# Kernel tuning notes

Measured on AMD Instinct MI355X. Metric: run time of the kernel, lower is better.

## Reference

```python
import jax, jax.numpy as jnp
import numpy as np

N, E, D, L, G, C = 20000, 320000, 512, 6, 64, 10
EPS = 1e-5


def setup_inputs() -> dict:
    key = jax.random.key(0)
    ks = jax.random.split(key, 8)
    s = 0.05  # small init scale to keep activations sane across 6 layers
    x = jax.random.normal(ks[0], (N, D), jnp.float32)
    edge_index = jax.random.randint(ks[1], (2, E), 0, N, jnp.int32)
    batch = jnp.sort(jax.random.randint(ks[2], (N,), 0, G, jnp.int32))
    W_rel = jax.random.normal(ks[3], (L, D, D), jnp.float32) * s
    b_rel = jnp.zeros((L, D), jnp.float32)
    W_root = jax.random.normal(ks[4], (L, D, D), jnp.float32) * s
    gamma = jnp.ones((L, D), jnp.float32)
    beta = jnp.zeros((L, D), jnp.float32)
    lin_w = jax.random.normal(ks[5], (D, C), jnp.float32) * s
    lin_b = jnp.zeros((C,), jnp.float32)
    return {"x": x, "edge_index": edge_index, "batch": batch,
            "W_rel": W_rel, "b_rel": b_rel, "W_root": W_root,
            "gamma": gamma, "beta": beta, "lin_w": lin_w, "lin_b": lin_b}


def reference(x, edge_index, batch, W_rel, b_rel, W_root, gamma, beta, lin_w, lin_b):
    # PyG GraphConv (aggr='add'): out = segment_sum(x[src] -> dst) @ W_rel + b_rel + x @ W_root
    src, dst = edge_index[0], edge_index[1]
    n = x.shape[0]
    for l in range(W_rel.shape[0]):  # 6 structurally identical layers
        agg = jax.ops.segment_sum(x[src], dst, num_segments=n)  # [N, D]
        h = agg @ W_rel[l] + b_rel[l] + x @ W_root[l]
        # BatchNorm1d in training mode: biased batch statistics over nodes
        mu = jnp.mean(h, axis=0)
        var = jnp.mean(jnp.square(h - mu), axis=0)
        x = jax.nn.relu((h - mu) * jax.lax.rsqrt(var + EPS) * gamma[l] + beta[l])
    # global_mean_pool over per-node graph ids
    sums = jax.ops.segment_sum(x, batch, num_segments=G)              # [G, D]
    counts = jax.ops.segment_sum(jnp.ones((n,), x.dtype), batch, num_segments=G)
    pooled = sums / jnp.maximum(counts, 1.0)[:, None]
    return pooled @ lin_w + lin_b  # [G, C]
```

## Files before the change

### kernel.cpp

```cpp
#include <hip/hip_runtime.h>


typedef unsigned short u16;
typedef unsigned int u32;
typedef __attribute__((ext_vector_type(8))) short bf16x8;
typedef __attribute__((ext_vector_type(16))) float f32x16;

#define DFEAT 512
#define KDIM 1024
#define NLAYER 6
#define NGRAPH 64
#define NCLS 10
#define BN_EPS 1e-5f

__device__ __forceinline__ float bf_lo(u32 u) { union { u32 i; float f; } v; v.i = u << 16; return v.f; }
__device__ __forceinline__ float bf_hi(u32 u) { union { u32 i; float f; } v; v.i = u & 0xFFFF0000u; return v.f; }
__device__ __forceinline__ u16 f2bf(float f) {
  union { float f; u32 i; } v; v.f = f;
  u32 r = v.i + 0x7FFFu + ((v.i >> 16) & 1u);
  return (u16)(r >> 16);
}
__device__ __forceinline__ u32 pack2(float lo, float hi) {
  return (u32)f2bf(lo) | ((u32)f2bf(hi) << 16);
}

__device__ __forceinline__ void gload_lds16(const u16* g, u16* lds_base) {
  __builtin_amdgcn_global_load_lds(
      (const __attribute__((address_space(1))) u32*)g,
      (__attribute__((address_space(3))) u32*)lds_base, 16, 0, 0);
}

__global__ void hist_kernel(const int* __restrict__ ei, int* __restrict__ counts, int E) {
  int e = blockIdx.x * 256 + threadIdx.x;
  if (e < E) atomicAdd(&counts[ei[E + e]], 1);
}

__global__ __launch_bounds__(1024) void scan_kernel(const int* __restrict__ counts,
                                                    int* __restrict__ row_ptr, int n) {
  __shared__ int buf[1024];
  int tid = threadIdx.x;
  int carry = 0;
  for (int base = 0; base < n; base += 1024) {
    int i = base + tid;
    int v = (i < n) ? counts[i] : 0;
    buf[tid] = v;
    __syncthreads();
    int x = v;
    for (int off = 1; off < 1024; off <<= 1) {
      int t = (tid >= off) ? buf[tid - off] : 0;
      __syncthreads();
      x += t;
      buf[tid] = x;
      __syncthreads();
    }
    if (i < n) row_ptr[i] = carry + x - v;
    int tot = buf[1023];
    __syncthreads();
    carry += tot;
  }
  if (tid == 0) row_ptr[n] = carry;
}

__global__ void scatter_kernel(const int* __restrict__ ei, int* __restrict__ cursor,
                               int* __restrict__ csr_src, int E) {
  int e = blockIdx.x * 256 + threadIdx.x;
  if (e < E) {
    int d = ei[E + e];
    int pos = atomicAdd(&cursor[d], 1);
    csr_src[pos] = ei[e];
  }
}

__global__ void wconv_kernel(const float* __restrict__ Wrel, const float* __restrict__ Wroot,
                             u16* __restrict__ Wt) {
  int idx = blockIdx.x * 256 + threadIdx.x;
  int k = idx & 1023;
  int n = (idx >> 10) & 511;
  int l = idx >> 19;
  float v = (k < DFEAT) ? Wrel[((size_t)l * DFEAT + k) * DFEAT + n]
                        : Wroot[((size_t)l * DFEAT + (k - DFEAT)) * DFEAT + n];
  Wt[idx] = f2bf(v);
}

__global__ void xconv_kernel(const float* __restrict__ x, u16* __restrict__ A, int M) {
  int idx = blockIdx.x * 256 + threadIdx.x;
  int row = idx >> 7;
  int c4 = (idx & 127) * 4;
  if (row >= M) return;
  float4 v = *(const float4*)&x[(size_t)row * DFEAT + c4];
  uint2 o; o.x = pack2(v.x, v.y); o.y = pack2(v.z, v.w);
  *(uint2*)&A[(size_t)row * KDIM + DFEAT + c4] = o;
}

__device__ __forceinline__ void add8(uint4 v, float* a) {
  a[0] += bf_lo(v.x); a[1] += bf_hi(v.x);
  a[2] += bf_lo(v.y); a[3] += bf_hi(v.y);
  a[4] += bf_lo(v.z); a[5] += bf_hi(v.z);
  a[6] += bf_lo(v.w); a[7] += bf_hi(v.w);
}

#define GCAP 1536
__global__ __launch_bounds__(256) void gather_kernel(u16* __restrict__ A,
                                                     const int* __restrict__ row_ptr,
                                                     const int* __restrict__ csr_src, int n) {
  __shared__ int sidx[GCAP];
  int b = blockIdx.x;
  int slice = b & 7;
  int grp = b >> 3;
  int tid = threadIdx.x;
  int r0 = grp * 32;
  int rend = (r0 + 32 < n) ? (r0 + 32) : n;
  int wbeg = row_ptr[r0], wend = row_ptr[rend];
  int cnt = wend - wbeg;
  bool lds_ok = (cnt <= GCAP);
  if (lds_ok)
    for (int t = tid; t < cnt; t += 256) sidx[t] = csr_src[wbeg + t];
  __syncthreads();

  int wid = tid >> 6, lane = tid & 63;
  int dsub = lane >> 3, fl = lane & 7;
  int dst = r0 + wid * 8 + dsub;
  if (dst >= n) return;
  int cc = slice * 64 + fl * 8;
  const u16* Sx = A + DFEAT + cc;
  int db = row_ptr[dst], de = row_ptr[dst + 1];
  float a[8] = {};
  if (lds_ok) {
    int e = db - wbeg, ee = de - wbeg;
    for (; e + 7 < ee; e += 8) {
      int s0 = sidx[e + 0], s1 = sidx[e + 1], s2 = sidx[e + 2], s3 = sidx[e + 3];
      int s4 = sidx[e + 4], s5 = sidx[e + 5], s6 = sidx[e + 6], s7 = sidx[e + 7];
      uint4 v0 = *(const uint4*)&Sx[(size_t)s0 * KDIM];
      uint4 v1 = *(const uint4*)&Sx[(size_t)s1 * KDIM];
      uint4 v2 = *(const uint4*)&Sx[(size_t)s2 * KDIM];
      uint4 v3 = *(const uint4*)&Sx[(size_t)s3 * KDIM];
      uint4 v4 = *(const uint4*)&Sx[(size_t)s4 * KDIM];
      uint4 v5 = *(const uint4*)&Sx[(size_t)s5 * KDIM];
      uint4 v6 = *(const uint4*)&Sx[(size_t)s6 * KDIM];
      uint4 v7 = *(const uint4*)&Sx[(size_t)s7 * KDIM];
      add8(v0, a); add8(v1, a); add8(v2, a); add8(v3, a);
      add8(v4, a); add8(v5, a); add8(v6, a); add8(v7, a);
    }
    for (; e < ee; ++e) {
      uint4 v = *(const uint4*)&Sx[(size_t)sidx[e] * KDIM];
      add8(v, a);
    }
  } else {
    for (int e = db; e < de; ++e) {
      uint4 v = *(const uint4*)&Sx[(size_t)csr_src[e] * KDIM];
      add8(v, a);
    }
  }
  uint4 o;
  o.x = pack2(a[0], a[1]); o.y = pack2(a[2], a[3]);
  o.z = pack2(a[4], a[5]); o.w = pack2(a[6], a[7]);
  *(uint4*)&A[(size_t)dst * KDIM + cc] = o;
}

#define BM 128
#define BN 128
#define BK 64
#define CSTR 132
__global__ __launch_bounds__(256, 4) void gemm_kernel(const u16* __restrict__ A,
                                                      const u16* __restrict__ Bt,
                                                      const float* __restrict__ bias,
                                                      u16* __restrict__ Hb,
                                                      float* __restrict__ sums, int M) {
  const int lin = blockIdx.x;
  const int bx = ((lin >> 5) << 3) + (lin & 7);
  const int by = (lin >> 3) & 3;
  const int m0 = bx * BM;
  if (m0 >= M) return;
  const int n0 = by * BN;

  __shared__ u16 smem[BM * CSTR];
  __shared__ float sred[2 * BN];
  u16* As = smem;
  u16* Bs = smem + BM * BK;
  const int tid = threadIdx.x;
  const int wid = tid >> 6, lane = tid & 63;
  const int wm = wid >> 1, wn = wid & 1;
  const int l31 = lane & 31, half = lane >> 5;

  if (tid < 2 * BN) sred[tid] = 0.f;

  const int dr = lane >> 3;
  const int gcol = ((lane & 7) ^ dr) * 8;
  int arow[4], brow[4];
#pragma unroll
  for (int t = 0; t < 4; t++) {
    int r = wid * 32 + t * 8 + dr;
    int ar = m0 + r; if (ar >= M) ar = M - 1;
    arow[t] = ar;
    brow[t] = n0 + r;
  }

  f32x16 acc[2][2] = {};

  for (int k0 = 0; k0 < KDIM; k0 += BK) {
    __syncthreads();
#pragma unroll
    for (int t = 0; t < 4; t++)
      gload_lds16(&A[(size_t)arow[t] * KDIM + k0 + gcol], &As[(wid * 32 + t * 8) * BK]);
#pragma unroll
    for (int t = 0; t < 4; t++)
      gload_lds16(&Bt[(size_t)brow[t] * KDIM + k0 + gcol], &Bs[(wid * 32 + t * 8) * BK]);
    __syncthreads();
#pragma unroll
    for (int ks = 0; ks < 4; ks++) {
      int slot = ((ks * 2 + half) ^ (l31 & 7)) * 8;
      bf16x8 a0 = *(const bf16x8*)&As[(wm * 64 + l31) * BK + slot];
      bf16x8 a1 = *(const bf16x8*)&As[(wm * 64 + 32 + l31) * BK + slot];
      bf16x8 b0 = *(const bf16x8*)&Bs[(wn * 64 + l31) * BK + slot];
      bf16x8 b1 = *(const bf16x8*)&Bs[(wn * 64 + 32 + l31) * BK + slot];
      acc[0][0] = __builtin_amdgcn_mfma_f32_32x32x16_bf16(a0, b0, acc[0][0], 0, 0, 0);
      acc[0][1] = __builtin_amdgcn_mfma_f32_32x32x16_bf16(a0, b1, acc[0][1], 0, 0, 0);
      acc[1][0] = __builtin_amdgcn_mfma_f32_32x32x16_bf16(a1, b0, acc[1][0], 0, 0, 0);
      acc[1][1] = __builtin_amdgcn_mfma_f32_32x32x16_bf16(a1, b1, acc[1][1], 0, 0, 0);
    }
  }

  __syncthreads();

#pragma unroll
  for (int nt = 0; nt < 2; nt++) {
    int colt = wn * 64 + nt * 32 + l31;
    float bv = bias[n0 + colt];
    float s = 0.f, s2 = 0.f;
#pragma unroll
    for (int mt = 0; mt < 2; mt++) {
      int rbase = wm * 64 + mt * 32 + half * 4;
#pragma unroll
      for (int reg = 0; reg < 16; reg++) {
        int rowt = rbase + (reg & 3) + 8 * (reg >> 2);
        float v = acc[mt][nt][reg] + bv;
        smem[rowt * CSTR + colt] = f2bf(v);
        if (m0 + rowt < M) { s += v; s2 += v * v; }
      }
    }
    s  += __shfl_xor(s, 32);
    s2 += __shfl_xor(s2, 32);
    if (half == 0) {
      atomicAdd(&sred[colt], s);
      atomicAdd(&sred[BN + colt], s2);
    }
  }
  __syncthreads();

  const int rsub = tid >> 4;
  const int c8 = (tid & 15) * 8;
#pragma unroll
  for (int it = 0; it < 8; it++) {
    int rowt = it * 16 + rsub;
    int grow = m0 + rowt;
    if (grow < M) {
      uint4 v = *(const uint4*)&smem[rowt * CSTR + c8];
      *(uint4*)&Hb[(size_t)grow * DFEAT + n0 + c8] = v;
    }
  }
  if (tid < BN) {
    atomicAdd(&sums[n0 + tid], sred[tid]);
    atomicAdd(&sums[DFEAT + n0 + tid], sred[BN + tid]);
  }
}

__global__ void norm_kernel(const u16* __restrict__ Hb, const float* __restrict__ sums,
                            const float* __restrict__ gamma, const float* __restrict__ beta,
                            u16* __restrict__ A, int M, float invN) {
  int idx = blockIdx.x * 256 + threadIdx.x;
  int row = idx >> 6;
  int c8 = (idx & 63) * 8;
  if (row >= M) return;
  float sc[8], sh[8];
#pragma unroll
  for (int j = 0; j < 8; j++) {
    int c = c8 + j;
    float mu = sums[c] * invN;
    float var = sums[DFEAT + c] * invN - mu * mu;
    float s = gamma[c] * rsqrtf(var + BN_EPS);
    sc[j] = s;
    sh[j] = beta[c] - mu * s;
  }
  uint4 h = *(const uint4*)&Hb[(size_t)row * DFEAT + c8];
  float x0 = fmaxf(bf_lo(h.x) * sc[0] + sh[0], 0.f);
  float x1 = fmaxf(bf_hi(h.x) * sc[1] + sh[1], 0.f);
  float x2 = fmaxf(bf_lo(h.y) * sc[2] + sh[2], 0.f);
  float x3 = fmaxf(bf_hi(h.y) * sc[3] + sh[3], 0.f);
  float x4 = fmaxf(bf_lo(h.z) * sc[4] + sh[4], 0.f);
  float x5 = fmaxf(bf_hi(h.z) * sc[5] + sh[5], 0.f);
  float x6 = fmaxf(bf_lo(h.w) * sc[6] + sh[6], 0.f);
  float x7 = fmaxf(bf_hi(h.w) * sc[7] + sh[7], 0.f);
  uint4 o; o.x = pack2(x0, x1); o.y = pack2(x2, x3);
  o.z = pack2(x4, x5); o.w = pack2(x6, x7);
  *(uint4*)&A[(size_t)row * KDIM + DFEAT + c8] = o;
}

__device__ __forceinline__ int lower_bound_dev(const int* a, int n, int v) {
  int lo = 0, hi = n;
  while (lo < hi) { int mid = (lo + hi) >> 1; if (a[mid] < v) lo = mid + 1; else hi = mid; }
  return lo;
}

__global__ __launch_bounds__(1024) void pool_kernel(const u16* __restrict__ Hb,
                                                    const float* __restrict__ sums,
                                                    const float* __restrict__ gamma,
                                                    const float* __restrict__ beta,
                                                    const int* __restrict__ batch,
                                                    float* __restrict__ pooled, int n, float invN) {
  __shared__ float red[DFEAT];
  int g = blockIdx.x;
  int tid = threadIdx.x;
  if (tid < DFEAT) red[tid] = 0.f;
  int lo = lower_bound_dev(batch, n, g);
  int hi = lower_bound_dev(batch, n, g + 1);
  int rowOff = tid >> 6, lane = tid & 63;
  int c0 = lane * 8;
  float sc[8], sh[8];
#pragma unroll
  for (int j = 0; j < 8; j++) {
    int c = c0 + j;
    float mu = sums[c] * invN;
    float var = sums[DFEAT + c] * invN - mu * mu;
    float s = gamma[c] * rsqrtf(var + BN_EPS);
    sc[j] = s;
    sh[j] = beta[c] - mu * s;
  }
  float a[8] = {};
  for (int r = lo + rowOff; r < hi; r += 16) {
    uint4 v = *(const uint4*)&Hb[(size_t)r * DFEAT + c0];
    float e0 = bf_lo(v.x), e1 = bf_hi(v.x), e2 = bf_lo(v.y), e3 = bf_hi(v.y);
    float e4 = bf_lo(v.z), e5 = bf_hi(v.z), e6 = bf_lo(v.w), e7 = bf_hi(v.w);
    a[0] += fmaxf(e0 * sc[0] + sh[0], 0.f); a[1] += fmaxf(e1 * sc[1] + sh[1], 0.f);
    a[2] += fmaxf(e2 * sc[2] + sh[2], 0.f); a[3] += fmaxf(e3 * sc[3] + sh[3], 0.f);
    a[4] += fmaxf(e4 * sc[4] + sh[4], 0.f); a[5] += fmaxf(e5 * sc[5] + sh[5], 0.f);
    a[6] += fmaxf(e6 * sc[6] + sh[6], 0.f); a[7] += fmaxf(e7 * sc[7] + sh[7], 0.f);
  }
  __syncthreads();
#pragma unroll
  for (int j = 0; j < 8; j++) atomicAdd(&red[c0 + j], a[j]);
  __syncthreads();
  if (tid < DFEAT) pooled[g * DFEAT + tid] = red[tid] / fmaxf((float)(hi - lo), 1.0f);
}

__global__ __launch_bounds__(64) void final_kernel(const float* __restrict__ pooled,
                                                   const float* __restrict__ lin_w,
                                                   const float* __restrict__ lin_b,
                                                   float* __restrict__ out) {
  int g = blockIdx.x;
  int lane = threadIdx.x;
  float acc[NCLS] = {};
  float4 p0 = *(const float4*)&pooled[g * DFEAT + lane * 8];
  float4 p1 = *(const float4*)&pooled[g * DFEAT + lane * 8 + 4];
  float pv[8] = {p0.x, p0.y, p0.z, p0.w, p1.x, p1.y, p1.z, p1.w};
#pragma unroll
  for (int j = 0; j < 8; j++) {
    int k = lane * 8 + j;
#pragma unroll
    for (int c = 0; c < NCLS; c++) acc[c] += pv[j] * lin_w[k * NCLS + c];
  }
#pragma unroll
  for (int off = 32; off > 0; off >>= 1)
#pragma unroll
    for (int c = 0; c < NCLS; c++) acc[c] += __shfl_down(acc[c], off);
  if (lane == 0)
#pragma unroll
    for (int c = 0; c < NCLS; c++) out[g * NCLS + c] = acc[c] + lin_b[c];
}

extern "C" void kernel_launch(void* const* d_in, const int* in_sizes, int n_in,
                              void* d_out, int out_size, void* d_ws, size_t ws_size,
                              hipStream_t stream) {
  const float* x      = (const float*)d_in[0];
  const int*   ei     = (const int*)d_in[1];
  const int*   batch  = (const int*)d_in[2];
  const float* W_rel  = (const float*)d_in[3];
  const float* b_rel  = (const float*)d_in[4];
  const float* W_root = (const float*)d_in[5];
  const float* gamma  = (const float*)d_in[6];
  const float* beta   = (const float*)d_in[7];
  const float* lin_w  = (const float*)d_in[8];
  const float* lin_b  = (const float*)d_in[9];
  float* out = (float*)d_out;

  const int N = in_sizes[0] / DFEAT;
  const int E = in_sizes[1] / 2;

  char* p = (char*)d_ws;
  u16*   A       = (u16*)p;    p += (size_t)N * KDIM * 2;
  u16*   Hb      = (u16*)p;    p += (size_t)N * DFEAT * 2;
  u16*   Wt      = (u16*)p;    p += (size_t)NLAYER * DFEAT * KDIM * 2;
  int*   row_ptr = (int*)p;    p += ((size_t)(N + 1) * 4 + 15) / 16 * 16;
  int*   cursor  = (int*)p;    p += (size_t)N * 4;
  int*   csr_src = (int*)p;    p += (size_t)E * 4;
  float* sums    = (float*)p;  p += (size_t)NLAYER * 2 * DFEAT * 4;
  float* pooled  = (float*)p;  p += (size_t)NGRAPH * DFEAT * 4;

  const float invN = 1.0f / (float)N;

  hipMemsetAsync(cursor, 0, (size_t)N * 4, stream);
  hipMemsetAsync(sums, 0, (size_t)NLAYER * 2 * DFEAT * 4, stream);

  hist_kernel<<<(E + 255) / 256, 256, 0, stream>>>(ei, cursor, E);
  scan_kernel<<<1, 1024, 0, stream>>>(cursor, row_ptr, N);
  hipMemcpyAsync(cursor, row_ptr, (size_t)N * 4, hipMemcpyDeviceToDevice, stream);
  scatter_kernel<<<(E + 255) / 256, 256, 0, stream>>>(ei, cursor, csr_src, E);

  wconv_kernel<<<(NLAYER * DFEAT * KDIM) / 256, 256, 0, stream>>>(W_rel, W_root, Wt);
  xconv_kernel<<<(N * 128 + 255) / 256, 256, 0, stream>>>(x, A, N);

  const int ngrp = (N + 31) / 32;
  const int gather_grid = ngrp * 8;
  const int gemm_rows = (N + BM - 1) / BM;
  const int gemm_grid = ((gemm_rows + 7) / 8) * 8 * 4;

  for (int l = 0; l < NLAYER; ++l) {
    float* sums_l = sums + (size_t)l * 2 * DFEAT;
    gather_kernel<<<gather_grid, 256, 0, stream>>>(A, row_ptr, csr_src, N);
    gemm_kernel<<<gemm_grid, 256, 0, stream>>>(A, Wt + (size_t)l * DFEAT * KDIM,
                                               b_rel + (size_t)l * DFEAT, Hb, sums_l, N);
    if (l < NLAYER - 1)
      norm_kernel<<<(N * 64 + 255) / 256, 256, 0, stream>>>(
          Hb, sums_l, gamma + (size_t)l * DFEAT, beta + (size_t)l * DFEAT, A, N, invN);
  }

  pool_kernel<<<NGRAPH, 1024, 0, stream>>>(Hb, sums + (size_t)(NLAYER - 1) * 2 * DFEAT,
                                           gamma + (size_t)(NLAYER - 1) * DFEAT,
                                           beta + (size_t)(NLAYER - 1) * DFEAT,
                                           batch, pooled, N, invN);
  final_kernel<<<NGRAPH, 64, 0, stream>>>(pooled, lin_w, lin_b, out);
}
```

Measured before the change: 613.1 us.

## Fuse per-layer gather/GEMM/norm/pool into one cooperative persistent kernel

Replaces the roughly twenty per-layer kernel launches with one cooperative persistent kernel. It loops over the gather, GEMM, norm, pool and final stages with grid-wide syncs between them, removing launch gaps and per-launch tail effects. The scan kernel now uses a chunked single-pass prefix sum and writes the cursor directly, which drops the device-to-device memcpy. The cost is a grid-stride schedule with occupancy capped at 3 blocks per CU, plus grid.sync overhead. The pool stage moves to 256-thread blocks and only 64 blocks do that work, so the pool tail may be slower.

```diff
diff --git a/kernel.cpp b/kernel.cpp
--- a/kernel.cpp
+++ b/kernel.cpp
@@ -1,4 +1,7 @@
 #include <hip/hip_runtime.h>
+#include <hip/hip_cooperative_groups.h>
+
+namespace cg = cooperative_groups;
 
 
 typedef unsigned short u16;
@@ -12,6 +15,12 @@
 #define NGRAPH 64
 #define NCLS 10
 #define BN_EPS 1e-5f
+#define GCAP 1536
+#define BM 128
+#define BN 128
+#define BK 64
+#define CSTR 132
+#define SHBYTES (BM * CSTR * 2 + 2 * BN * 4)
 
 __device__ __forceinline__ float bf_lo(u32 u) { union { u32 i; float f; } v; v.i = u << 16; return v.f; }
 __device__ __forceinline__ float bf_hi(u32 u) { union { u32 i; float f; } v; v.i = u & 0xFFFF0000u; return v.f; }
@@ -35,30 +44,38 @@
   if (e < E) atomicAdd(&counts[ei[E + e]], 1);
 }
 
+#define SCHUNK 20
 __global__ __launch_bounds__(1024) void scan_kernel(const int* __restrict__ counts,
-                                                    int* __restrict__ row_ptr, int n) {
-  __shared__ int buf[1024];
+                                                    int* __restrict__ row_ptr,
+                                                    int* __restrict__ cursor, int n) {
+  __shared__ int part[1024];
   int tid = threadIdx.x;
-  int carry = 0;
-  for (int base = 0; base < n; base += 1024) {
-    int i = base + tid;
-    int v = (i < n) ? counts[i] : 0;
-    buf[tid] = v;
+  int base = tid * SCHUNK;
+  int loc[SCHUNK];
+  int s = 0;
+#pragma unroll
+  for (int i = 0; i < SCHUNK; i++) {
+    int idx = base + i;
+    int v = (idx < n) ? counts[idx] : 0;
+    loc[i] = s; s += v;
+  }
+  part[tid] = s;
+  __syncthreads();
+  int x = s;
+  for (int off = 1; off < 1024; off <<= 1) {
+    int t = (tid >= off) ? part[tid - off] : 0;
     __syncthreads();
-    int x = v;
-    for (int off = 1; off < 1024; off <<= 1) {
-      int t = (tid >= off) ? buf[tid - off] : 0;
-      __syncthreads();
-      x += t;
-      buf[tid] = x;
-      __syncthreads();
-    }
-    if (i < n) row_ptr[i] = carry + x - v;
-    int tot = buf[1023];
+    x += t;
+    part[tid] = x;
     __syncthreads();
-    carry += tot;
-  }
-  if (tid == 0) row_ptr[n] = carry;
+  }
+  int offset = x - s;
+#pragma unroll
+  for (int i = 0; i < SCHUNK; i++) {
+    int idx = base + i;
+    if (idx < n) { int v = offset + loc[i]; row_ptr[idx] = v; cursor[idx] = v; }
+  }
+  if (tid == 1023) row_ptr[n] = offset + s;
 }
 
 __global__ void scatter_kernel(const int* __restrict__ ei, int* __restrict__ cursor,
@@ -99,20 +116,19 @@
   a[6] += bf_lo(v.w); a[7] += bf_hi(v.w);
 }
 
-#define GCAP 1536
-__global__ __launch_bounds__(256) void gather_kernel(u16* __restrict__ A,
-                                                     const int* __restrict__ row_ptr,
-                                                     const int* __restrict__ csr_src, int n) {
-  __shared__ int sidx[GCAP];
-  int b = blockIdx.x;
-  int slice = b & 7;
-  int grp = b >> 3;
+__device__ __forceinline__ void gather_body(int vb, u16* __restrict__ A,
+                                            const int* __restrict__ row_ptr,
+                                            const int* __restrict__ csr_src, int n,
+                                            int* sidx) {
+  int slice = vb & 7;
+  int grp = vb >> 3;
   int tid = threadIdx.x;
   int r0 = grp * 32;
   int rend = (r0 + 32 < n) ? (r0 + 32) : n;
   int wbeg = row_ptr[r0], wend = row_ptr[rend];
   int cnt = wend - wbeg;
   bool lds_ok = (cnt <= GCAP);
+  __syncthreads();
   if (lds_ok)
     for (int t = tid; t < cnt; t += 256) sidx[t] = csr_src[wbeg + t];
   __syncthreads();
@@ -120,61 +136,53 @@
   int wid = tid >> 6, lane = tid & 63;
   int dsub = lane >> 3, fl = lane & 7;
   int dst = r0 + wid * 8 + dsub;
-  if (dst >= n) return;
-  int cc = slice * 64 + fl * 8;
-  const u16* Sx = A + DFEAT + cc;
-  int db = row_ptr[dst], de = row_ptr[dst + 1];
-  float a[8] = {};
-  if (lds_ok) {
-    int e = db - wbeg, ee = de - wbeg;
-    for (; e + 7 < ee; e += 8) {
-      int s0 = sidx[e + 0], s1 = sidx[e + 1], s2 = sidx[e + 2], s3 = sidx[e + 3];
-      int s4 = sidx[e + 4], s5 = sidx[e + 5], s6 = sidx[e + 6], s7 = sidx[e + 7];
-      uint4 v0 = *(const uint4*)&Sx[(size_t)s0 * KDIM];
-      uint4 v1 = *(const uint4*)&Sx[(size_t)s1 * KDIM];
-      uint4 v2 = *(const uint4*)&Sx[(size_t)s2 * KDIM];
-      uint4 v3 = *(const uint4*)&Sx[(size_t)s3 * KDIM];
-      uint4 v4 = *(const uint4*)&Sx[(size_t)s4 * KDIM];
-      uint4 v5 = *(const uint4*)&Sx[(size_t)s5 * KDIM];
-      uint4 v6 = *(const uint4*)&Sx[(size_t)s6 * KDIM];
-      uint4 v7 = *(const uint4*)&Sx[(size_t)s7 * KDIM];
-      add8(v0, a); add8(v1, a); add8(v2, a); add8(v3, a);
-      add8(v4, a); add8(v5, a); add8(v6, a); add8(v7, a);
-    }
-    for (; e < ee; ++e) {
-      uint4 v = *(const uint4*)&Sx[(size_t)sidx[e] * KDIM];
-      add8(v, a);
-    }
-  } else {
-    for (int e = db; e < de; ++e) {
-      uint4 v = *(const uint4*)&Sx[(size_t)csr_src[e] * KDIM];
-      add8(v, a);
-    }
-  }
-  uint4 o;
-  o.x = pack2(a[0], a[1]); o.y = pack2(a[2], a[3]);
-  o.z = pack2(a[4], a[5]); o.w = pack2(a[6], a[7]);
-  *(uint4*)&A[(size_t)dst * KDIM + cc] = o;
-}
-
-#define BM 128
-#define BN 128
-#define BK 64
-#define CSTR 132
-__global__ __launch_bounds__(256, 4) void gemm_kernel(const u16* __restrict__ A,
-                                                      const u16* __restrict__ Bt,
-                                                      const float* __restrict__ bias,
-                                                      u16* __restrict__ Hb,
-                                                      float* __restrict__ sums, int M) {
-  const int lin = blockIdx.x;
+  if (dst < n) {
+    int cc = slice * 64 + fl * 8;
+    const u16* Sx = A + DFEAT + cc;
+    int db = row_ptr[dst], de = row_ptr[dst + 1];
+    float a[8] = {};
+    if (lds_ok) {
+      int e = db - wbeg, ee = de - wbeg;
+      for (; e + 7 < ee; e += 8) {
+        int s0 = sidx[e + 0], s1 = sidx[e + 1], s2 = sidx[e + 2], s3 = sidx[e + 3];
+        int s4 = sidx[e + 4], s5 = sidx[e + 5], s6 = sidx[e + 6], s7 = sidx[e + 7];
+        uint4 v0 = *(const uint4*)&Sx[(size_t)s0 * KDIM];
+        uint4 v1 = *(const uint4*)&Sx[(size_t)s1 * KDIM];
+        uint4 v2 = *(const uint4*)&Sx[(size_t)s2 * KDIM];
+        uint4 v3 = *(const uint4*)&Sx[(size_t)s3 * KDIM];
+        uint4 v4 = *(const uint4*)&Sx[(size_t)s4 * KDIM];
+        uint4 v5 = *(const uint4*)&Sx[(size_t)s5 * KDIM];
+        uint4 v6 = *(const uint4*)&Sx[(size_t)s6 * KDIM];
+        uint4 v7 = *(const uint4*)&Sx[(size_t)s7 * KDIM];
+        add8(v0, a); add8(v1, a); add8(v2, a); add8(v3, a);
+        add8(v4, a); add8(v5, a); add8(v6, a); add8(v7, a);
+      }
+      for (; e < ee; ++e) {
+        uint4 v = *(const uint4*)&Sx[(size_t)sidx[e] * KDIM];
+        add8(v, a);
+      }
+    } else {
+      for (int e = db; e < de; ++e) {
+        uint4 v = *(const uint4*)&Sx[(size_t)csr_src[e] * KDIM];
+        add8(v, a);
+      }
+    }
+    uint4 o;
+    o.x = pack2(a[0], a[1]); o.y = pack2(a[2], a[3]);
+    o.z = pack2(a[4], a[5]); o.w = pack2(a[6], a[7]);
+    *(uint4*)&A[(size_t)dst * KDIM + cc] = o;
+  }
+}
+
+__device__ void gemm_body(int lin, const u16* __restrict__ A, const u16* __restrict__ Bt,
+                          const float* __restrict__ bias, u16* __restrict__ Hb,
+                          float* __restrict__ sums, int M, u16* smem, float* sred) {
   const int bx = ((lin >> 5) << 3) + (lin & 7);
   const int by = (lin >> 3) & 3;
   const int m0 = bx * BM;
   if (m0 >= M) return;
   const int n0 = by * BN;
 
-  __shared__ u16 smem[BM * CSTR];
-  __shared__ float sred[2 * BN];
   u16* As = smem;
   u16* Bs = smem + BM * BK;
   const int tid = threadIdx.x;
@@ -264,10 +272,11 @@
   }
 }
 
-__global__ void norm_kernel(const u16* __restrict__ Hb, const float* __restrict__ sums,
-                            const float* __restrict__ gamma, const float* __restrict__ beta,
-                            u16* __restrict__ A, int M, float invN) {
-  int idx = blockIdx.x * 256 + threadIdx.x;
+__device__ __forceinline__ void norm_body(int idx, const u16* __restrict__ Hb,
+                                          const float* __restrict__ sums,
+                                          const float* __restrict__ gamma,
+                                          const float* __restrict__ beta,
+                                          u16* __restrict__ A, int M, float invN) {
   int row = idx >> 6;
   int c8 = (idx & 63) * 8;
   if (row >= M) return;
@@ -301,16 +310,12 @@
   return lo;
 }
 
-__global__ __launch_bounds__(1024) void pool_kernel(const u16* __restrict__ Hb,
-                                                    const float* __restrict__ sums,
-                                                    const float* __restrict__ gamma,
-                                                    const float* __restrict__ beta,
-                                                    const int* __restrict__ batch,
-                                                    float* __restrict__ pooled, int n, float invN) {
-  __shared__ float red[DFEAT];
-  int g = blockIdx.x;
+__device__ void pool_body(int g, const u16* __restrict__ Hb, const float* __restrict__ sums,
+                          const float* __restrict__ gamma, const float* __restrict__ beta,
+                          const int* __restrict__ batch, float* __restrict__ pooled,
+                          int n, float invN, float* red) {
   int tid = threadIdx.x;
-  if (tid < DFEAT) red[tid] = 0.f;
+  red[tid] = 0.f; red[tid + 256] = 0.f;
   int lo = lower_bound_dev(batch, n, g);
   int hi = lower_bound_dev(batch, n, g + 1);
   int rowOff = tid >> 6, lane = tid & 63;
@@ -326,7 +331,7 @@
     sh[j] = beta[c] - mu * s;
   }
   float a[8] = {};
-  for (int r = lo + rowOff; r < hi; r += 16) {
+  for (int r = lo + rowOff; r < hi; r += 4) {
     uint4 v = *(const uint4*)&Hb[(size_t)r * DFEAT + c0];
     float e0 = bf_lo(v.x), e1 = bf_hi(v.x), e2 = bf_lo(v.y), e3 = bf_hi(v.y);
     float e4 = bf_lo(v.z), e5 = bf_hi(v.z), e6 = bf_lo(v.w), e7 = bf_hi(v.w);
@@ -339,32 +344,114 @@
 #pragma unroll
   for (int j = 0; j < 8; j++) atomicAdd(&red[c0 + j], a[j]);
   __syncthreads();
-  if (tid < DFEAT) pooled[g * DFEAT + tid] = red[tid] / fmaxf((float)(hi - lo), 1.0f);
-}
-
-__global__ __launch_bounds__(64) void final_kernel(const float* __restrict__ pooled,
-                                                   const float* __restrict__ lin_w,
-                                                   const float* __restrict__ lin_b,
-                                                   float* __restrict__ out) {
-  int g = blockIdx.x;
-  int lane = threadIdx.x;
-  float acc[NCLS] = {};
-  float4 p0 = *(const float4*)&pooled[g * DFEAT + lane * 8];
-  float4 p1 = *(const float4*)&pooled[g * DFEAT + lane * 8 + 4];
-  float pv[8] = {p0.x, p0.y, p0.z, p0.w, p1.x, p1.y, p1.z, p1.w};
-#pragma unroll
-  for (int j = 0; j < 8; j++) {
-    int k = lane * 8 + j;
-#pragma unroll
-    for (int c = 0; c < NCLS; c++) acc[c] += pv[j] * lin_w[k * NCLS + c];
-  }
-#pragma unroll
-  for (int off = 32; off > 0; off >>= 1)
-#pragma unroll
-    for (int c = 0; c < NCLS; c++) acc[c] += __shfl_down(acc[c], off);
-  if (lane == 0)
-#pragma unroll
-    for (int c = 0; c < NCLS; c++) out[g * NCLS + c] = acc[c] + lin_b[c];
+  float cnt = fmaxf((float)(hi - lo), 1.0f);
+  pooled[g * DFEAT + tid] = red[tid] / cnt;
+  pooled[g * DFEAT + tid + 256] = red[tid + 256] / cnt;
+  __syncthreads();
+}
+
+__device__ void final_body(const float* __restrict__ pooled, const float* __restrict__ lin_w,
+                           const float* __restrict__ lin_b, float* __restrict__ out) {
+  int tid = threadIdx.x;
+  if (tid >= 64) return;
+  for (int g = 0; g < NGRAPH; ++g) {
+    float acc[NCLS] = {};
+    float4 p0 = *(const float4*)&pooled[g * DFEAT + tid * 8];
+    float4 p1 = *(const float4*)&pooled[g * DFEAT + tid * 8 + 4];
+    float pv[8] = {p0.x, p0.y, p0.z, p0.w, p1.x, p1.y, p1.z, p1.w};
+#pragma unroll
+    for (int j = 0; j < 8; j++) {
+      int k = tid * 8 + j;
+#pragma unroll
+      for (int c = 0; c < NCLS; c++) acc[c] += pv[j] * lin_w[k * NCLS + c];
+    }
+#pragma unroll
+    for (int off = 32; off > 0; off >>= 1)
+#pragma unroll
+      for (int c = 0; c < NCLS; c++) acc[c] += __shfl_down(acc[c], off);
+    if (tid == 0)
+#pragma unroll
+      for (int c = 0; c < NCLS; c++) out[g * NCLS + c] = acc[c] + lin_b[c];
+  }
+}
+
+__global__ __launch_bounds__(256, 3) void fused_layers(
+    u16* A, u16* Hb, const u16* Wt, const float* b_rel,
+    const float* gamma, const float* beta,
+    const int* row_ptr, const int* csr_src, float* sums,
+    const int* batch, float* pooled, const float* lin_w, const float* lin_b,
+    float* out, int N, float invN) {
+  __shared__ __align__(16) char shbuf[SHBYTES];
+  cg::grid_group grid = cg::this_grid();
+  const int nb = gridDim.x;
+  const int ngrp8 = ((N + 31) / 32) * 8;
+  const int gtiles = (((N + BM - 1) / BM + 7) / 8) * 8 * 4;
+  const int nvb = (N * 64 + 255) / 256;
+  int* sidx = (int*)shbuf;
+  u16* smem = (u16*)shbuf;
+  float* sred = (float*)(shbuf + BM * CSTR * 2);
+  float* red = (float*)shbuf;
+
+  for (int l = 0; l < NLAYER; ++l) {
+    for (int vb = blockIdx.x; vb < ngrp8; vb += nb)
+      gather_body(vb, A, row_ptr, csr_src, N, sidx);
+    grid.sync();
+
+    const u16* Bt = Wt + (size_t)l * DFEAT * KDIM;
+    const float* bias = b_rel + (size_t)l * DFEAT;
+    float* sums_l = sums + (size_t)l * 2 * DFEAT;
+    for (int vb = blockIdx.x; vb < gtiles; vb += nb) {
+      gemm_body(vb, A, Bt, bias, Hb, sums_l, N, smem, sred);
+      __syncthreads();
+    }
+    grid.sync();
+
+    if (l < NLAYER - 1) {
+      const float* g_l = gamma + (size_t)l * DFEAT;
+      const float* be_l = beta + (size_t)l * DFEAT;
+      for (int vb = blockIdx.x; vb < nvb; vb += nb)
+        norm_body(vb * 256 + (int)threadIdx.x, Hb, sums_l, g_l, be_l, A, N, invN);
+      grid.sync();
+    }
+  }
+
+  const float* sums_last = sums + (size_t)(NLAYER - 1) * 2 * DFEAT;
+  for (int g = blockIdx.x; g < NGRAPH; g += nb)
+    pool_body(g, Hb, sums_last, gamma + (size_t)(NLAYER - 1) * DFEAT,
+              beta + (size_t)(NLAYER - 1) * DFEAT, batch, pooled, N, invN, red);
+  grid.sync();
+  if (blockIdx.x == 0) final_body(pooled, lin_w, lin_b, out);
+}
+
+__global__ __launch_bounds__(256) void gather_kernel(u16* A, const int* row_ptr,
+                                                     const int* csr_src, int n) {
+  __shared__ int sidx[GCAP];
+  gather_body(blockIdx.x, A, row_ptr, csr_src, n, sidx);
+}
+
+__global__ __launch_bounds__(256, 4) void gemm_kernel(const u16* A, const u16* Bt,
+                                                      const float* bias, u16* Hb,
+                                                      float* sums, int M) {
+  __shared__ __align__(16) char shb[SHBYTES];
+  gemm_body(blockIdx.x, A, Bt, bias, Hb, sums, M, (u16*)shb, (float*)(shb + BM * CSTR * 2));
+}
+
+__global__ void norm_kernel(const u16* Hb, const float* sums, const float* gamma,
+                            const float* beta, u16* A, int M, float invN) {
+  norm_body(blockIdx.x * 256 + (int)threadIdx.x, Hb, sums, gamma, beta, A, M, invN);
+}
+
+__global__ __launch_bounds__(256) void pool_kernel(const u16* Hb, const float* sums,
+                                                   const float* gamma, const float* beta,
+                                                   const int* batch, float* pooled,
+                                                   int n, float invN) {
+  __shared__ float red[DFEAT];
+  pool_body(blockIdx.x, Hb, sums, gamma, beta, batch, pooled, n, invN, red);
+}
+
+__global__ __launch_bounds__(64) void final_kernel(const float* pooled, const float* lin_w,
+                                                   const float* lin_b, float* out) {
+  final_body(pooled, lin_w, lin_b, out);
 }
 
 extern "C" void kernel_launch(void* const* d_in, const int* in_sizes, int n_in,
@@ -401,31 +488,51 @@
   hipMemsetAsync(sums, 0, (size_t)NLAYER * 2 * DFEAT * 4, stream);
 
   hist_kernel<<<(E + 255) / 256, 256, 0, stream>>>(ei, cursor, E);
-  scan_kernel<<<1, 1024, 0, stream>>>(cursor, row_ptr, N);
-  hipMemcpyAsync(cursor, row_ptr, (size_t)N * 4, hipMemcpyDeviceToDevice, stream);
+  scan_kernel<<<1, 1024, 0, stream>>>(cursor, row_ptr, cursor, N);
   scatter_kernel<<<(E + 255) / 256, 256, 0, stream>>>(ei, cursor, csr_src, E);
 
   wconv_kernel<<<(NLAYER * DFEAT * KDIM) / 256, 256, 0, stream>>>(W_rel, W_root, Wt);
   xconv_kernel<<<(N * 128 + 255) / 256, 256, 0, stream>>>(x, A, N);
 
-  const int ngrp = (N + 31) / 32;
-  const int gather_grid = ngrp * 8;
-  const int gemm_rows = (N + BM - 1) / BM;
-  const int gemm_grid = ((gemm_rows + 7) / 8) * 8 * 4;
-
-  for (int l = 0; l < NLAYER; ++l) {
-    float* sums_l = sums + (size_t)l * 2 * DFEAT;
-    gather_kernel<<<gather_grid, 256, 0, stream>>>(A, row_ptr, csr_src, N);
-    gemm_kernel<<<gemm_grid, 256, 0, stream>>>(A, Wt + (size_t)l * DFEAT * KDIM,
-                                               b_rel + (size_t)l * DFEAT, Hb, sums_l, N);
-    if (l < NLAYER - 1)
-      norm_kernel<<<(N * 64 + 255) / 256, 256, 0, stream>>>(
-          Hb, sums_l, gamma + (size_t)l * DFEAT, beta + (size_t)l * DFEAT, A, N, invN);
-  }
-
-  pool_kernel<<<NGRAPH, 1024, 0, stream>>>(Hb, sums + (size_t)(NLAYER - 1) * 2 * DFEAT,
-                                           gamma + (size_t)(NLAYER - 1) * DFEAT,
-                                           beta + (size_t)(NLAYER - 1) * DFEAT,
-                                           batch, pooled, N, invN);
-  final_kernel<<<NGRAPH, 64, 0, stream>>>(pooled, lin_w, lin_b, out);
-}
+  int maxB = 0;
+  hipError_t occErr = hipOccupancyMaxActiveBlocksPerMultiprocessor(&maxB, fused_layers, 256, 0);
+  int grid = 0;
+  if (occErr == hipSuccess && maxB > 0) {
+    grid = maxB * 256;
+    if (grid > 1024) grid = 1024;
+    grid &= ~7;
+  }
+  bool coop_done = false;
+  if (grid >= 256) {
+    u16* A_ = A; u16* Hb_ = Hb; const u16* Wt_ = Wt;
+    const float* br_ = b_rel; const float* g_ = gamma; const float* be_ = beta;
+    const int* rp_ = row_ptr; const int* cs_ = csr_src; float* su_ = sums;
+    const int* ba_ = batch; float* po_ = pooled;
+    const float* lw_ = lin_w; const float* lb_ = lin_b; float* out_ = out;
+    int N_ = N; float invN_ = invN;
+    void* args[] = {&A_, &Hb_, &Wt_, &br_, &g_, &be_, &rp_, &cs_, &su_,
+                    &ba_, &po_, &lw_, &lb_, &out_, &N_, &invN_};
+    hipError_t e = hipLaunchCooperativeKernel((const void*)fused_layers,
+                                              dim3(grid), dim3(256), args, 0, stream);
+    coop_done = (e == hipSuccess);
+  }
+
+  if (!coop_done) {
+    const int ngrp8 = ((N + 31) / 32) * 8;
+    const int gtiles = (((N + BM - 1) / BM + 7) / 8) * 8 * 4;
+    for (int l = 0; l < NLAYER; ++l) {
+      float* sums_l = sums + (size_t)l * 2 * DFEAT;
+      gather_kernel<<<ngrp8, 256, 0, stream>>>(A, row_ptr, csr_src, N);
+      gemm_kernel<<<gtiles, 256, 0, stream>>>(A, Wt + (size_t)l * DFEAT * KDIM,
+                                              b_rel + (size_t)l * DFEAT, Hb, sums_l, N);
+      if (l < NLAYER - 1)
+        norm_kernel<<<(N * 64 + 255) / 256, 256, 0, stream>>>(
+            Hb, sums_l, gamma + (size_t)l * DFEAT, beta + (size_t)l * DFEAT, A, N, invN);
+    }
+    pool_kernel<<<NGRAPH, 256, 0, stream>>>(Hb, sums + (size_t)(NLAYER - 1) * 2 * DFEAT,
+                                            gamma + (size_t)(NLAYER - 1) * DFEAT,
+                                            beta + (size_t)(NLAYER - 1) * DFEAT,
+                                            batch, pooled, N, invN);
+    final_kernel<<<1, 64, 0, stream>>>(pooled, lin_w, lin_b, out);
+  }
+}
```

After: 1.865 ms. +204.1%, slower.
